# Kernel optimization log

Measured on AMD Instinct MI355X. Metric: run time of the kernel, lower is better.

The kernel has to match this reference:

```python
import jax, jax.numpy as jnp
import numpy as np

# PCEN constants (from __init__ defaults)
ALPHA = 0.98
DELTA = 2.0
R = 0.5
S = 0.025
EPS = 1e-6


def setup_inputs() -> dict:
    key = jax.random.key(0)
    # mel spectrogram energies: [batch, mel_bins, time], nonnegative
    x = jax.random.uniform(key, (64, 128, 4096), dtype=jnp.float32)
    return {"x": x}


def _ema_smooth(x):
    # x: [B, C, T]. smooth[0] = x[0]; smooth[t] = (1-S)*smooth[t-1] + S*x[t]
    x_t = jnp.moveaxis(x, -1, 0)  # [T, B, C]
    init = x_t[0]

    def step(carry, xt):
        sm = (1.0 - S) * carry + S * xt
        return sm, sm

    _, rest = jax.lax.scan(step, init, x_t[1:])  # [T-1, B, C]
    smooth = jnp.concatenate([init[None], rest], axis=0)  # [T, B, C]
    return jnp.moveaxis(smooth, 0, -1)  # [B, C, T]


def reference(x):
    smooth = _ema_smooth(x)
    return (x / (smooth + EPS) ** ALPHA + DELTA) ** R - DELTA ** R
```

## Files before the change

kernel.cpp:

```cpp
#include <hip/hip_runtime.h>
#include <math.h>


#define T_LEN 4096
#define BLOCK 256
#define PER   16
#define NWAVE (BLOCK / 64)

__global__ __launch_bounds__(BLOCK) void pcen_kernel(const float* __restrict__ x,
                                                     float* __restrict__ out) {
    constexpr float A_COEF = 0.975f;
    constexpr float S_COEF = 0.025f;
    constexpr float ALPHA  = 0.98f;
    constexpr float EPS    = 1e-6f;
    constexpr float DELTA  = 2.0f;
    constexpr float SQRT_DELTA = 1.4142135623730951f;
    constexpr float A16 =
        0.975f*0.975f*0.975f*0.975f*0.975f*0.975f*0.975f*0.975f*
        0.975f*0.975f*0.975f*0.975f*0.975f*0.975f*0.975f*0.975f;

    const int row = blockIdx.x;
    const float* __restrict__ xr  = x   + (size_t)row * T_LEN;
    float* __restrict__       orr = out + (size_t)row * T_LEN;

    const int tid  = threadIdx.x;
    const int base = tid * PER;

    float xv[PER];
    {
        float4 v0 = *(const float4*)(xr + base);
        float4 v1 = *(const float4*)(xr + base + 4);
        float4 v2 = *(const float4*)(xr + base + 8);
        float4 v3 = *(const float4*)(xr + base + 12);
        xv[0]=v0.x; xv[1]=v0.y; xv[2]=v0.z;  xv[3]=v0.w;
        xv[4]=v1.x; xv[5]=v1.y; xv[6]=v1.z;  xv[7]=v1.w;
        xv[8]=v2.x; xv[9]=v2.y; xv[10]=v2.z; xv[11]=v2.w;
        xv[12]=v3.x; xv[13]=v3.y; xv[14]=v3.z; xv[15]=v3.w;
    }

    float Bi[PER];
    float A;
    if (tid == 0) { Bi[0] = xv[0];          A = 0.0f; }
    else          { Bi[0] = S_COEF * xv[0]; A = A16;  }
#pragma unroll
    for (int i = 1; i < PER; ++i) {
        Bi[i] = fmaf(A_COEF, Bi[i-1], S_COEF * xv[i]);
    }
    float B = Bi[PER-1];

    const int lane = tid & 63;
#pragma unroll
    for (int off = 1; off < 64; off <<= 1) {
        float Au = __shfl_up(A, off);
        float Bu = __shfl_up(B, off);
        if (lane >= off) {
            B = fmaf(A, Bu, B);
            A = A * Au;
        }
    }

    __shared__ float wA[NWAVE], wB[NWAVE];
    const int wid = tid >> 6;
    if (lane == 63) { wA[wid] = A; wB[wid] = B; }
    __syncthreads();

    float Aex = __shfl_up(A, 1);
    float Bex = __shfl_up(B, 1);
    if (lane == 0) { Aex = 1.0f; Bex = 0.0f; }

    float WB = 0.0f;
    for (int w = 0; w < wid; ++w) {
        WB = fmaf(wA[w], WB, wB[w]);
    }

    float y_in = fmaf(Aex, WB, Bex);

    float ap = A_COEF;
#pragma unroll
    for (int i = 0; i < PER; ++i) {
        float sm = fmaf(ap, y_in, Bi[i]);
        ap *= A_COEF;
        float p = __builtin_amdgcn_exp2f(-ALPHA * __builtin_amdgcn_logf(sm + EPS));
        xv[i] = __builtin_amdgcn_sqrtf(fmaf(xv[i], p, DELTA)) - SQRT_DELTA;
    }

    {
        float4 v0, v1, v2, v3;
        v0.x=xv[0];  v0.y=xv[1];  v0.z=xv[2];  v0.w=xv[3];
        v1.x=xv[4];  v1.y=xv[5];  v1.z=xv[6];  v1.w=xv[7];
        v2.x=xv[8];  v2.y=xv[9];  v2.z=xv[10]; v2.w=xv[11];
        v3.x=xv[12]; v3.y=xv[13]; v3.z=xv[14]; v3.w=xv[15];
        *(float4*)(orr + base)      = v0;
        *(float4*)(orr + base + 4)  = v1;
        *(float4*)(orr + base + 8)  = v2;
        *(float4*)(orr + base + 12) = v3;
    }
}

extern "C" void kernel_launch(void* const* d_in, const int* in_sizes, int n_in,
                              void* d_out, int out_size, void* d_ws, size_t ws_size,
                              hipStream_t stream) {
    const float* x = (const float*)d_in[0];
    float* out = (float*)d_out;
    const int rows = in_sizes[0] / T_LEN;
    pcen_kernel<<<rows, BLOCK, 0, stream>>>(x, out);
}
```

Baseline: 233.7 us.

## Stage row loads and stores through swizzled LDS for coalesced global access

Global loads and stores now use a fully coalesced pattern, with consecutive threads touching consecutive float4s, and are staged through a 16KB shared-memory buffer. An XOR swizzle is meant to avoid bank conflicts when each thread reads its contiguous 16-element chunk back out. The aim is better global memory efficiency than the earlier layout, where each thread read a strided 64-byte chunk. The cost is two extra barriers and LDS traffic, plus higher LDS use per block, which may lower occupancy.

```diff
diff --git a/kernel.cpp b/kernel.cpp
--- a/kernel.cpp
+++ b/kernel.cpp
@@ -6,6 +6,10 @@
 #define BLOCK 256
 #define PER   16
 #define NWAVE (BLOCK / 64)
+
+__device__ __forceinline__ int swz(int a) {
+    return a ^ (((a >> 7) & 7) << 2);
+}
 
 __global__ __launch_bounds__(BLOCK) void pcen_kernel(const float* __restrict__ x,
                                                      float* __restrict__ out) {
@@ -19,23 +23,28 @@
         0.975f*0.975f*0.975f*0.975f*0.975f*0.975f*0.975f*0.975f*
         0.975f*0.975f*0.975f*0.975f*0.975f*0.975f*0.975f*0.975f;
 
+    __shared__ float lds[T_LEN];
+    __shared__ float wA[NWAVE], wB[NWAVE];
+
     const int row = blockIdx.x;
     const float* __restrict__ xr  = x   + (size_t)row * T_LEN;
     float* __restrict__       orr = out + (size_t)row * T_LEN;
+    const int tid = threadIdx.x;
 
-    const int tid  = threadIdx.x;
-    const int base = tid * PER;
+#pragma unroll
+    for (int c = 0; c < 4; ++c) {
+        const int a = tid * 4 + c * 1024;
+        float4 v = *(const float4*)(xr + a);
+        *(float4*)(&lds[swz(a)]) = v;
+    }
+    __syncthreads();
 
     float xv[PER];
-    {
-        float4 v0 = *(const float4*)(xr + base);
-        float4 v1 = *(const float4*)(xr + base + 4);
-        float4 v2 = *(const float4*)(xr + base + 8);
-        float4 v3 = *(const float4*)(xr + base + 12);
-        xv[0]=v0.x; xv[1]=v0.y; xv[2]=v0.z;  xv[3]=v0.w;
-        xv[4]=v1.x; xv[5]=v1.y; xv[6]=v1.z;  xv[7]=v1.w;
-        xv[8]=v2.x; xv[9]=v2.y; xv[10]=v2.z; xv[11]=v2.w;
-        xv[12]=v3.x; xv[13]=v3.y; xv[14]=v3.z; xv[15]=v3.w;
+#pragma unroll
+    for (int j = 0; j < 4; ++j) {
+        const int a = tid * PER + j * 4;
+        float4 v = *(const float4*)(&lds[swz(a)]);
+        xv[j*4+0] = v.x; xv[j*4+1] = v.y; xv[j*4+2] = v.z; xv[j*4+3] = v.w;
     }
 
     float Bi[PER];
@@ -59,7 +68,6 @@
         }
     }
 
-    __shared__ float wA[NWAVE], wB[NWAVE];
     const int wid = tid >> 6;
     if (lane == 63) { wA[wid] = A; wB[wid] = B; }
     __syncthreads();
@@ -72,7 +80,6 @@
     for (int w = 0; w < wid; ++w) {
         WB = fmaf(wA[w], WB, wB[w]);
     }
-
     float y_in = fmaf(Aex, WB, Bex);
 
     float ap = A_COEF;
@@ -84,16 +91,20 @@
         xv[i] = __builtin_amdgcn_sqrtf(fmaf(xv[i], p, DELTA)) - SQRT_DELTA;
     }
 
-    {
-        float4 v0, v1, v2, v3;
-        v0.x=xv[0];  v0.y=xv[1];  v0.z=xv[2];  v0.w=xv[3];
-        v1.x=xv[4];  v1.y=xv[5];  v1.z=xv[6];  v1.w=xv[7];
-        v2.x=xv[8];  v2.y=xv[9];  v2.z=xv[10]; v2.w=xv[11];
-        v3.x=xv[12]; v3.y=xv[13]; v3.z=xv[14]; v3.w=xv[15];
-        *(float4*)(orr + base)      = v0;
-        *(float4*)(orr + base + 4)  = v1;
-        *(float4*)(orr + base + 8)  = v2;
-        *(float4*)(orr + base + 12) = v3;
+#pragma unroll
+    for (int j = 0; j < 4; ++j) {
+        const int a = tid * PER + j * 4;
+        float4 v;
+        v.x = xv[j*4+0]; v.y = xv[j*4+1]; v.z = xv[j*4+2]; v.w = xv[j*4+3];
+        *(float4*)(&lds[swz(a)]) = v;
+    }
+    __syncthreads();
+
+#pragma unroll
+    for (int c = 0; c < 4; ++c) {
+        const int a = tid * 4 + c * 1024;
+        float4 v = *(const float4*)(&lds[swz(a)]);
+        *(float4*)(orr + a) = v;
     }
 }
 
```

Measured after the change: 227.4 us. 1.03x faster.
